# Kernel optimization log

Measured on AMD Instinct MI355X. Metric: run time of the kernel, lower is better.

Reference implementation:

```python
import jax, jax.numpy as jnp
import numpy as np

D_MODEL = 1024
NUM_HEADS = 16
HEAD_DIM = D_MODEL // NUM_HEADS  # 64


def setup_inputs() -> dict:
    key = jax.random.key(0)
    k1, k2, k3 = jax.random.split(key, 3)
    x = jax.random.normal(k1, (4, 2048, D_MODEL), dtype=jnp.float32)
    w_qkv = jax.random.normal(k2, (3 * D_MODEL, D_MODEL), dtype=jnp.float32) * 0.02
    b_qkv = jnp.zeros((3 * D_MODEL,), dtype=jnp.float32)
    w_out = jax.random.normal(k3, (D_MODEL, D_MODEL), dtype=jnp.float32) * 0.02
    b_out = jnp.zeros((D_MODEL,), dtype=jnp.float32)
    return {"x": x, "w_qkv": w_qkv, "b_qkv": b_qkv, "w_out": w_out, "b_out": b_out}


def reference(x, w_qkv, b_qkv, w_out, b_out):
    N, S, _ = x.shape
    # qkv projection: (N, S, 3*D) -> (3, N, heads, S, head_dim), matching torch permute(2,0,3,1,4)
    qkv = (jnp.einsum('nsd,ed->nse', x, w_qkv) + b_qkv)
    qkv = qkv.reshape(N, S, 3, NUM_HEADS, HEAD_DIM).transpose(2, 0, 3, 1, 4)
    queries, keys, values = qkv[0], qkv[1], qkv[2]  # each (N, heads, S, head_dim)
    # Faithful to source: einsum labels axis1 as 'q'/'k' and axis2 as 'h',
    # so energy has shape (N, S, heads, heads) -- attention over the heads axis.
    energy = jnp.einsum('nqhd,nkhd->nhqk', queries, keys)
    attention = jax.nn.softmax(energy / jnp.sqrt(jnp.float32(HEAD_DIM)), axis=3)
    out = jnp.einsum('nhql,nlhd->nqhd', attention, values).reshape(N, S, D_MODEL)
    return jnp.einsum('nsd,od->nso', out, w_out) + b_out
```

## Files before the change

### kernel.cpp

```cpp
#include <hip/hip_runtime.h>
#include <hip/hip_bf16.h>


typedef __hip_bfloat16 bf16;
using bf16x8 = __attribute__((ext_vector_type(8))) short;
using f32x4  = __attribute__((ext_vector_type(4))) float;

__device__ __forceinline__ float b2f(unsigned short u) {
    return __uint_as_float(((unsigned)u) << 16);
}
__device__ __forceinline__ unsigned short f2b(float f) {
    bf16 h = __float2bfloat16(f);
    return *reinterpret_cast<unsigned short*>(&h);
}
__device__ __forceinline__ void store1(float* p, float v) { *p = v; }
__device__ __forceinline__ void store1(bf16* p, float v) { *p = __float2bfloat16(v); }

__device__ __forceinline__ void gload_lds16(const bf16* g, bf16* l) {
    __builtin_amdgcn_global_load_lds(
        (const __attribute__((address_space(1))) void*)g,
        (__attribute__((address_space(3))) void*)l, 16, 0, 0);
}

#define BAR()   __builtin_amdgcn_s_barrier()
#define LGKM(N) asm volatile("s_waitcnt lgkmcnt(" #N ")" ::: "memory")
#define VMC(N)  asm volatile("s_waitcnt vmcnt(" #N ")" ::: "memory")

template <typename CT>
__global__ __launch_bounds__(512, 2)
void gemm3p(const bf16* __restrict__ A, const bf16* __restrict__ B,
            const float* __restrict__ bias, CT* __restrict__ C,
            int M, int N, int K, int gx) {
    __shared__ alignas(1024) bf16 smem[3][384 * 64];

    const int t    = threadIdx.x;
    const int lane = t & 63;
    const int wid  = t >> 6;
    const int wr   = wid >> 2;
    const int wc   = wid & 3;

    const int nwg = gridDim.x;
    const int bid = blockIdx.x;
    const int wg  = (bid & 7) * (nwg >> 3) + (bid >> 3);
    const int m0  = (wg / gx) * 128;
    const int n0  = (wg % gx) * 256;

    const int nt = K / 64;

    const int srow = lane >> 3;
    const int kel  = ((lane & 7) ^ (lane >> 3)) * 8;

    auto stageA = [&](int tt) {
        if (tt >= nt) return;
        bf16* lp = &smem[tt % 3][wid * 1024];
        const bf16* gp = A + (size_t)(m0 + wid * 16 + srow) * K + tt * 64 + kel;
        gload_lds16(gp, lp);
        gload_lds16(gp + (size_t)8 * K, lp + 512);
    };
    auto stageB = [&](int tt, int h) {
        if (tt >= nt) return;
        bf16* lp = &smem[tt % 3][8192 + h * 8192 + wid * 1024];
        const bf16* gp = B + (size_t)(n0 + h * 128 + wid * 16 + srow) * K + tt * 64 + kel;
        gload_lds16(gp, lp);
        gload_lds16(gp + (size_t)8 * K, lp + 512);
    };

    const int arow_base = wr * 64 + (lane & 15);
    const int brow_base = wc * 64 + (lane & 15);
    const int kqb       = (lane >> 4) * 16;
    auto LDA = [&](int buf, int kk, int m) -> bf16x8 {
        const int row = arow_base + m * 16;
        const int ab  = row * 128 + ((kk * 64 + kqb) ^ ((row & 7) << 4));
        return *(const bf16x8*)((const char*)&smem[buf][0] + ab);
    };
    auto LDB = [&](int buf, int kk, int n) -> bf16x8 {
        const int row = brow_base + n * 16;
        const int bb  = 16384 + row * 128 + ((kk * 64 + kqb) ^ ((row & 7) << 4));
        return *(const bf16x8*)((const char*)&smem[buf][0] + bb);
    };

    f32x4 acc[4][4] = {};
    bf16x8 afc[4], bfc[4];
    bf16x8 afa[4], bfa[4];

    stageA(0); stageB(0, 0); stageB(0, 1);
    stageA(1); stageB(1, 0); stageB(1, 1);
    VMC(6);
    BAR();
#pragma unroll
    for (int m = 0; m < 4; ++m) afc[m] = LDA(0, 0, m);
#pragma unroll
    for (int n = 0; n < 4; ++n) bfc[n] = LDB(0, 0, n);

    for (int tt = 0; tt < nt; ++tt) {
        const int buf = tt % 3;

#pragma unroll
        for (int m = 0; m < 4; ++m) afa[m] = LDA(buf, 1, m);
#pragma unroll
        for (int n = 0; n < 4; ++n) bfa[n] = LDB(buf, 1, n);
        stageA(tt + 2); stageB(tt + 2, 0); stageB(tt + 2, 1);
        LGKM(8);
        __builtin_amdgcn_s_setprio(1);
#pragma unroll
        for (int m = 0; m < 4; ++m)
#pragma unroll
            for (int n = 0; n < 4; ++n)
                acc[m][n] = __builtin_amdgcn_mfma_f32_16x16x32_bf16(
                    afc[m], bfc[n], acc[m][n], 0, 0, 0);
        __builtin_amdgcn_s_setprio(0);
        if (tt < nt - 2) { VMC(6); } else { VMC(0); }
        BAR();
        if (tt + 1 < nt) {
            const int nb = (tt + 1) % 3;
#pragma unroll
            for (int m = 0; m < 4; ++m) afc[m] = LDA(nb, 0, m);
#pragma unroll
            for (int n = 0; n < 4; ++n) bfc[n] = LDB(nb, 0, n);
            LGKM(8);
        } else {
            LGKM(0);
        }
        __builtin_amdgcn_s_setprio(1);
#pragma unroll
        for (int m = 0; m < 4; ++m)
#pragma unroll
            for (int n = 0; n < 4; ++n)
                acc[m][n] = __builtin_amdgcn_mfma_f32_16x16x32_bf16(
                    afa[m], bfa[n], acc[m][n], 0, 0, 0);
        __builtin_amdgcn_s_setprio(0);
        BAR();
    }

#pragma unroll
    for (int m = 0; m < 4; ++m) {
        const int row = m0 + wr * 64 + m * 16 + (lane >> 4) * 4;
#pragma unroll
        for (int n = 0; n < 4; ++n) {
            const int col = n0 + wc * 64 + n * 16 + (lane & 15);
            const float bval = bias[col];
#pragma unroll
            for (int r = 0; r < 4; ++r)
                store1(&C[(size_t)(row + r) * N + col], acc[m][n][r] + bval);
        }
    }
}

__global__ __launch_bounds__(256)
void cvt_f32_bf16(const float* __restrict__ in, bf16* __restrict__ out, int n4) {
    int i = blockIdx.x * 256 + threadIdx.x;
    if (i >= n4) return;
    float4 v = ((const float4*)in)[i];
    ushort4 o = {f2b(v.x), f2b(v.y), f2b(v.z), f2b(v.w)};
    ((ushort4*)out)[i] = o;
}

__global__ __launch_bounds__(256)
void attn_kernel(const bf16* __restrict__ qkv, bf16* __restrict__ T) {
    __shared__ float lds[4][48 * 68];

    const int wave = threadIdx.x >> 6;
    const int lane = threadIdx.x & 63;
    const int token = blockIdx.x * 4 + wave;
    const int n = token >> 11;
    const int s = token & 2047;

    float* L = lds[wave];
    const bf16* src = qkv + (size_t)token * 3072;

#pragma unroll
    for (int i = 0; i < 6; ++i) {
        int idx = i * 64 + lane;
        uint4 v = *reinterpret_cast<const uint4*>(src + (size_t)idx * 8);
        int e0 = idx * 8;
        float* dst = &L[(e0 >> 6) * 68 + (e0 & 63)];
        float4 a, b;
        a.x = b2f((unsigned short)(v.x & 0xffff));
        a.y = b2f((unsigned short)(v.x >> 16));
        a.z = b2f((unsigned short)(v.y & 0xffff));
        a.w = b2f((unsigned short)(v.y >> 16));
        b.x = b2f((unsigned short)(v.z & 0xffff));
        b.y = b2f((unsigned short)(v.z >> 16));
        b.z = b2f((unsigned short)(v.w & 0xffff));
        b.w = b2f((unsigned short)(v.w >> 16));
        *(float4*)dst = a;
        *(float4*)(dst + 4) = b;
    }
    __syncthreads();

    const int q0 = lane & 15;
    const int g  = lane >> 4;

    float e[4] = {0.f, 0.f, 0.f, 0.f};
    const float* Qr = &L[q0 * 68];
    const float* K0 = &L[(16 + g * 4) * 68];
#pragma unroll
    for (int d = 0; d < 64; d += 4) {
        float4 q4 = *(const float4*)(Qr + d);
#pragma unroll
        for (int j = 0; j < 4; ++j) {
            float4 k4 = *(const float4*)(K0 + j * 68 + d);
            e[j] += q4.x * k4.x + q4.y * k4.y + q4.z * k4.z + q4.w * k4.w;
        }
    }
#pragma unroll
    for (int j = 0; j < 4; ++j) e[j] *= 0.125f;

    float m = fmaxf(fmaxf(e[0], e[1]), fmaxf(e[2], e[3]));
    m = fmaxf(m, __shfl_xor(m, 16));
    m = fmaxf(m, __shfl_xor(m, 32));
    float p[4], sum = 0.f;
#pragma unroll
    for (int j = 0; j < 4; ++j) { p[j] = __expf(e[j] - m); sum += p[j]; }
    sum += __shfl_xor(sum, 16);
    sum += __shfl_xor(sum, 32);
    const float inv = 1.0f / sum;

    float prow[16];
#pragma unroll
    for (int j = 0; j < 4; ++j) {
        prow[g * 4 + j]         = p[j] * inv;
        prow[((g ^ 1) * 4) + j] = __shfl_xor(p[j], 16) * inv;
        prow[((g ^ 2) * 4) + j] = __shfl_xor(p[j], 32) * inv;
        prow[((g ^ 3) * 4) + j] = __shfl_xor(p[j], 48) * inv;
    }

    const int d0 = g * 16;
    float4 o4[4] = {};
#pragma unroll
    for (int k = 0; k < 16; ++k) {
        const float p1 = prow[k];
        const float* Vr = &L[(32 + k) * 68 + d0];
#pragma unroll
        for (int c = 0; c < 4; ++c) {
            float4 v = *(const float4*)(Vr + c * 4);
            o4[c].x += p1 * v.x; o4[c].y += p1 * v.y;
            o4[c].z += p1 * v.z; o4[c].w += p1 * v.w;
        }
    }
    unsigned short outv[16];
#pragma unroll
    for (int c = 0; c < 4; ++c) {
        outv[c * 4 + 0] = f2b(o4[c].x); outv[c * 4 + 1] = f2b(o4[c].y);
        outv[c * 4 + 2] = f2b(o4[c].z); outv[c * 4 + 3] = f2b(o4[c].w);
    }
    const int sp = q0 * 128 + (s >> 4);
    size_t off = ((size_t)n * 2048 + sp) * 1024 + (size_t)(s & 15) * 64 + d0;
    uint4* dst = reinterpret_cast<uint4*>(T + off);
    const uint4* sv = reinterpret_cast<const uint4*>(outv);
    dst[0] = sv[0];
    dst[1] = sv[1];
}

extern "C" void kernel_launch(void* const* d_in, const int* in_sizes, int n_in,
                              void* d_out, int out_size, void* d_ws, size_t ws_size,
                              hipStream_t stream) {
    const float* x     = (const float*)d_in[0];
    const float* w_qkv = (const float*)d_in[1];
    const float* b_qkv = (const float*)d_in[2];
    const float* w_out = (const float*)d_in[3];
    const float* b_out = (const float*)d_in[4];
    float* out = (float*)d_out;

    const int M = 8192, E = 3072, K = 1024, D = 1024;

    bf16* qkv = (bf16*)d_ws;
    bf16* T   = qkv + (size_t)M * E;
    bf16* W2b = qkv;
    bf16* W1b = (bf16*)d_out;
    bf16* X16 = W1b + (size_t)E * K;

    dim3 blk(256);

    cvt_f32_bf16<<<dim3(M * K / 4 / 256), blk, 0, stream>>>(x, X16, M * K / 4);
    cvt_f32_bf16<<<dim3(E * K / 4 / 256), blk, 0, stream>>>(w_qkv, W1b, E * K / 4);
    gemm3p<bf16><<<dim3((M / 128) * (E / 256)), dim3(512), 0, stream>>>(
        X16, W1b, b_qkv, qkv, M, E, K, E / 256);
    attn_kernel<<<dim3(M / 4), blk, 0, stream>>>(qkv, T);
    cvt_f32_bf16<<<dim3(D * K / 4 / 256), blk, 0, stream>>>(w_out, W2b, D * K / 4);
    gemm3p<float><<<dim3((M / 128) * (D / 256)), dim3(512), 0, stream>>>(
        T, W2b, b_out, out, M, D, K, D / 256);
}
```

Measured before the change: 127.9 us.

## Use one barrier per K-tile in GEMM and fuse the two input conversions

The GEMM main loop is restructured from two half-steps, each with its own barrier, to a single step per K tile. That step loads both k-halves of A and B fragments from LDS up front, then issues two MFMA batches with one barrier at the end. This removes a barrier and the cross-iteration fragment prefetch, trading load/compute overlap for less synchronization and more registers. Separately, the x and w_qkv fp32-to-bf16 conversions are merged into one launch to save a kernel launch.

```diff
diff --git a/kernel.cpp b/kernel.cpp
--- a/kernel.cpp
+++ b/kernel.cpp
@@ -28,7 +28,7 @@
 
 template <typename CT>
 __global__ __launch_bounds__(512, 2)
-void gemm3p(const bf16* __restrict__ A, const bf16* __restrict__ B,
+void gemm1b(const bf16* __restrict__ A, const bf16* __restrict__ B,
             const float* __restrict__ bias, CT* __restrict__ C,
             int M, int N, int K, int gx) {
     __shared__ alignas(1024) bf16 smem[3][384 * 64];
@@ -80,25 +80,24 @@
     };
 
     f32x4 acc[4][4] = {};
-    bf16x8 afc[4], bfc[4];
-    bf16x8 afa[4], bfa[4];
+    bf16x8 af0[4], bf0[4], af1[4], bf1[4];
 
     stageA(0); stageB(0, 0); stageB(0, 1);
     stageA(1); stageB(1, 0); stageB(1, 1);
     VMC(6);
     BAR();
-#pragma unroll
-    for (int m = 0; m < 4; ++m) afc[m] = LDA(0, 0, m);
-#pragma unroll
-    for (int n = 0; n < 4; ++n) bfc[n] = LDB(0, 0, n);
 
     for (int tt = 0; tt < nt; ++tt) {
         const int buf = tt % 3;
 
 #pragma unroll
-        for (int m = 0; m < 4; ++m) afa[m] = LDA(buf, 1, m);
-#pragma unroll
-        for (int n = 0; n < 4; ++n) bfa[n] = LDB(buf, 1, n);
+        for (int m = 0; m < 4; ++m) af0[m] = LDA(buf, 0, m);
+#pragma unroll
+        for (int n = 0; n < 4; ++n) bf0[n] = LDB(buf, 0, n);
+#pragma unroll
+        for (int m = 0; m < 4; ++m) af1[m] = LDA(buf, 1, m);
+#pragma unroll
+        for (int n = 0; n < 4; ++n) bf1[n] = LDB(buf, 1, n);
         stageA(tt + 2); stageB(tt + 2, 0); stageB(tt + 2, 1);
         LGKM(8);
         __builtin_amdgcn_s_setprio(1);
@@ -107,29 +106,19 @@
 #pragma unroll
             for (int n = 0; n < 4; ++n)
                 acc[m][n] = __builtin_amdgcn_mfma_f32_16x16x32_bf16(
-                    afc[m], bfc[n], acc[m][n], 0, 0, 0);
+                    af0[m], bf0[n], acc[m][n], 0, 0, 0);
+        __builtin_amdgcn_s_setprio(0);
+        LGKM(0);
+        __builtin_amdgcn_s_setprio(1);
+#pragma unroll
+        for (int m = 0; m < 4; ++m)
+#pragma unroll
+            for (int n = 0; n < 4; ++n)
+                acc[m][n] = __builtin_amdgcn_mfma_f32_16x16x32_bf16(
+                    af1[m], bf1[n], acc[m][n], 0, 0, 0);
         __builtin_amdgcn_s_setprio(0);
         if (tt < nt - 2) { VMC(6); } else { VMC(0); }
         BAR();
-        if (tt + 1 < nt) {
-            const int nb = (tt + 1) % 3;
-#pragma unroll
-            for (int m = 0; m < 4; ++m) afc[m] = LDA(nb, 0, m);
-#pragma unroll
-            for (int n = 0; n < 4; ++n) bfc[n] = LDB(nb, 0, n);
-            LGKM(8);
-        } else {
-            LGKM(0);
-        }
-        __builtin_amdgcn_s_setprio(1);
-#pragma unroll
-        for (int m = 0; m < 4; ++m)
-#pragma unroll
-            for (int n = 0; n < 4; ++n)
-                acc[m][n] = __builtin_amdgcn_mfma_f32_16x16x32_bf16(
-                    afa[m], bfa[n], acc[m][n], 0, 0, 0);
-        __builtin_amdgcn_s_setprio(0);
-        BAR();
     }
 
 #pragma unroll
@@ -144,6 +133,19 @@
                 store1(&C[(size_t)(row + r) * N + col], acc[m][n][r] + bval);
         }
     }
+}
+
+__global__ __launch_bounds__(256)
+void cvt2_f32_bf16(const float* __restrict__ in1, bf16* __restrict__ out1, int n1,
+                   const float* __restrict__ in2, bf16* __restrict__ out2, int n2) {
+    int i = blockIdx.x * 256 + threadIdx.x;
+    const float* in;
+    bf16* out;
+    if (i < n1) { in = in1; out = out1; }
+    else        { in = in2; out = out2; i -= n1; if (i >= n2) return; }
+    float4 v = ((const float4*)in)[i];
+    ushort4 o = {f2b(v.x), f2b(v.y), f2b(v.z), f2b(v.w)};
+    ((ushort4*)out)[i] = o;
 }
 
 __global__ __launch_bounds__(256)
@@ -271,13 +273,14 @@
     bf16* X16 = W1b + (size_t)E * K;
 
     dim3 blk(256);
-
-    cvt_f32_bf16<<<dim3(M * K / 4 / 256), blk, 0, stream>>>(x, X16, M * K / 4);
-    cvt_f32_bf16<<<dim3(E * K / 4 / 256), blk, 0, stream>>>(w_qkv, W1b, E * K / 4);
-    gemm3p<bf16><<<dim3((M / 128) * (E / 256)), dim3(512), 0, stream>>>(
+    const int n1 = M * K / 4, n2 = E * K / 4;
+
+    cvt2_f32_bf16<<<dim3((n1 + n2) / 256), blk, 0, stream>>>(
+        x, X16, n1, w_qkv, W1b, n2);
+    gemm1b<bf16><<<dim3((M / 128) * (E / 256)), dim3(512), 0, stream>>>(
         X16, W1b, b_qkv, qkv, M, E, K, E / 256);
     attn_kernel<<<dim3(M / 4), blk, 0, stream>>>(qkv, T);
     cvt_f32_bf16<<<dim3(D * K / 4 / 256), blk, 0, stream>>>(w_out, W2b, D * K / 4);
-    gemm3p<float><<<dim3((M / 128) * (D / 256)), dim3(512), 0, stream>>>(
+    gemm1b<float><<<dim3((M / 128) * (D / 256)), dim3(512), 0, stream>>>(
         T, W2b, b_out, out, M, D, K, D / 256);
 }
```

Result: faster. 124.1 us (-3.0%).

## Fuse fp32-to-bf16 conversion of x into QKV GEMM A-tile staging

Applied to the files above, without the earlier changes.

Drops the standalone conversion kernel for x. The QKV GEMM now loads fp32 A rows into registers, converts them to bf16 and writes them into swizzled LDS one stage ahead, while B still uses direct global-to-LDS loads. The main loop is also restructured so both k-halves are read from LDS at the start of each iteration, with one barrier per iteration instead of two. This removes a full write and re-read of the bf16 copy of x, at the cost of twice the global bytes for A, extra VALU conversion work and register pressure inside the GEMM.

```diff
diff --git a/kernel.cpp b/kernel.cpp
--- a/kernel.cpp
+++ b/kernel.cpp
@@ -26,11 +26,11 @@
 #define LGKM(N) asm volatile("s_waitcnt lgkmcnt(" #N ")" ::: "memory")
 #define VMC(N)  asm volatile("s_waitcnt vmcnt(" #N ")" ::: "memory")
 
-template <typename CT>
+template <bool AFP32, typename CT>
 __global__ __launch_bounds__(512, 2)
-void gemm3p(const bf16* __restrict__ A, const bf16* __restrict__ B,
-            const float* __restrict__ bias, CT* __restrict__ C,
-            int M, int N, int K, int gx) {
+void gemmf(const void* __restrict__ Av, const bf16* __restrict__ B,
+           const float* __restrict__ bias, CT* __restrict__ C,
+           int M, int N, int K, int gx) {
     __shared__ alignas(1024) bf16 smem[3][384 * 64];
 
     const int t    = threadIdx.x;
@@ -44,25 +44,53 @@
     const int wg  = (bid & 7) * (nwg >> 3) + (bid >> 3);
     const int m0  = (wg / gx) * 128;
     const int n0  = (wg % gx) * 256;
-
-    const int nt = K / 64;
+    const int nt  = K / 64;
 
     const int srow = lane >> 3;
     const int kel  = ((lane & 7) ^ (lane >> 3)) * 8;
 
-    auto stageA = [&](int tt) {
-        if (tt >= nt) return;
-        bf16* lp = &smem[tt % 3][wid * 1024];
-        const bf16* gp = A + (size_t)(m0 + wid * 16 + srow) * K + tt * 64 + kel;
-        gload_lds16(gp, lp);
-        gload_lds16(gp + (size_t)8 * K, lp + 512);
-    };
     auto stageB = [&](int tt, int h) {
         if (tt >= nt) return;
         bf16* lp = &smem[tt % 3][8192 + h * 8192 + wid * 1024];
         const bf16* gp = B + (size_t)(n0 + h * 128 + wid * 16 + srow) * K + tt * 64 + kel;
         gload_lds16(gp, lp);
         gload_lds16(gp + (size_t)8 * K, lp + 512);
+    };
+    auto stageA16 = [&](int tt) {
+        if (tt >= nt) return;
+        const bf16* A = (const bf16*)Av;
+        bf16* lp = &smem[tt % 3][wid * 1024];
+        const bf16* gp = A + (size_t)(m0 + wid * 16 + srow) * K + tt * 64 + kel;
+        gload_lds16(gp, lp);
+        gload_lds16(gp + (size_t)8 * K, lp + 512);
+    };
+
+    const int arow = t >> 2;
+    const int akb0 = (t & 3) * 32;
+    float4 ar0, ar1, ar2, ar3;
+    auto aregLoad = [&](int tt) {
+        if (tt >= nt) return;
+        const float* A = (const float*)Av;
+        const float* gp = A + (size_t)(m0 + arow) * K + tt * 64 + (akb0 >> 1);
+        ar0 = ((const float4*)gp)[0];
+        ar1 = ((const float4*)gp)[1];
+        ar2 = ((const float4*)gp)[2];
+        ar3 = ((const float4*)gp)[3];
+    };
+    auto aWriteF = [&](int tt, float4 f0, float4 f1, float4 f2, float4 f3) {
+        char* base = (char*)&smem[tt % 3][0];
+        const int swz = (arow & 7) << 4;
+        uint4 w0, w1;
+        w0.x = (unsigned)f2b(f0.x) | ((unsigned)f2b(f0.y) << 16);
+        w0.y = (unsigned)f2b(f0.z) | ((unsigned)f2b(f0.w) << 16);
+        w0.z = (unsigned)f2b(f1.x) | ((unsigned)f2b(f1.y) << 16);
+        w0.w = (unsigned)f2b(f1.z) | ((unsigned)f2b(f1.w) << 16);
+        w1.x = (unsigned)f2b(f2.x) | ((unsigned)f2b(f2.y) << 16);
+        w1.y = (unsigned)f2b(f2.z) | ((unsigned)f2b(f2.w) << 16);
+        w1.z = (unsigned)f2b(f3.x) | ((unsigned)f2b(f3.y) << 16);
+        w1.w = (unsigned)f2b(f3.z) | ((unsigned)f2b(f3.w) << 16);
+        *(uint4*)(base + arow * 128 + (akb0 ^ swz))        = w0;
+        *(uint4*)(base + arow * 128 + ((akb0 + 16) ^ swz)) = w1;
     };
 
     const int arow_base = wr * 64 + (lane & 15);
@@ -80,26 +108,54 @@
     };
 
     f32x4 acc[4][4] = {};
-    bf16x8 afc[4], bfc[4];
-    bf16x8 afa[4], bfa[4];
-
-    stageA(0); stageB(0, 0); stageB(0, 1);
-    stageA(1); stageB(1, 0); stageB(1, 1);
-    VMC(6);
-    BAR();
-#pragma unroll
-    for (int m = 0; m < 4; ++m) afc[m] = LDA(0, 0, m);
-#pragma unroll
-    for (int n = 0; n < 4; ++n) bfc[n] = LDB(0, 0, n);
+    bf16x8 af0[4], bv0[4], af1[4], bv1[4];
+
+    if constexpr (AFP32) {
+        stageB(0, 0); stageB(0, 1); stageB(1, 0); stageB(1, 1);
+        const float* A = (const float*)Av;
+        const float* g0 = A + (size_t)(m0 + arow) * K + (akb0 >> 1);
+        const float* g1 = g0 + 64;
+        float4 p0 = ((const float4*)g0)[0], p1 = ((const float4*)g0)[1],
+               p2 = ((const float4*)g0)[2], p3 = ((const float4*)g0)[3];
+        float4 q0 = ((const float4*)g1)[0], q1 = ((const float4*)g1)[1],
+               q2 = ((const float4*)g1)[2], q3 = ((const float4*)g1)[3];
+        VMC(0);
+        aWriteF(0, p0, p1, p2, p3);
+        aWriteF(1, q0, q1, q2, q3);
+        aregLoad(2);
+        LGKM(0);
+        BAR();
+    } else {
+        stageA16(0); stageB(0, 0); stageB(0, 1);
+        stageA16(1); stageB(1, 0); stageB(1, 1);
+        VMC(6);
+        BAR();
+    }
 
     for (int tt = 0; tt < nt; ++tt) {
         const int buf = tt % 3;
 
 #pragma unroll
-        for (int m = 0; m < 4; ++m) afa[m] = LDA(buf, 1, m);
-#pragma unroll
-        for (int n = 0; n < 4; ++n) bfa[n] = LDB(buf, 1, n);
-        stageA(tt + 2); stageB(tt + 2, 0); stageB(tt + 2, 1);
+        for (int m = 0; m < 4; ++m) af0[m] = LDA(buf, 0, m);
+#pragma unroll
+        for (int n = 0; n < 4; ++n) bv0[n] = LDB(buf, 0, n);
+#pragma unroll
+        for (int m = 0; m < 4; ++m) af1[m] = LDA(buf, 1, m);
+#pragma unroll
+        for (int n = 0; n < 4; ++n) bv1[n] = LDB(buf, 1, n);
+        stageB(tt + 2, 0); stageB(tt + 2, 1);
+        if constexpr (AFP32) {
+            if (tt + 2 < nt) {
+                VMC(4);
+                aWriteF(tt + 2, ar0, ar1, ar2, ar3);
+                aregLoad(tt + 3);
+            } else {
+                VMC(0);
+            }
+        } else {
+            stageA16(tt + 2);
+        }
+
         LGKM(8);
         __builtin_amdgcn_s_setprio(1);
 #pragma unroll
@@ -107,17 +163,10 @@
 #pragma unroll
             for (int n = 0; n < 4; ++n)
                 acc[m][n] = __builtin_amdgcn_mfma_f32_16x16x32_bf16(
-                    afc[m], bfc[n], acc[m][n], 0, 0, 0);
+                    af0[m], bv0[n], acc[m][n], 0, 0, 0);
         __builtin_amdgcn_s_setprio(0);
-        if (tt < nt - 2) { VMC(6); } else { VMC(0); }
-        BAR();
-        if (tt + 1 < nt) {
-            const int nb = (tt + 1) % 3;
-#pragma unroll
-            for (int m = 0; m < 4; ++m) afc[m] = LDA(nb, 0, m);
-#pragma unroll
-            for (int n = 0; n < 4; ++n) bfc[n] = LDB(nb, 0, n);
-            LGKM(8);
+        if constexpr (AFP32) {
+            if (tt + 2 < nt) { LGKM(2); } else { LGKM(0); }
         } else {
             LGKM(0);
         }
@@ -127,8 +176,14 @@
 #pragma unroll
             for (int n = 0; n < 4; ++n)
                 acc[m][n] = __builtin_amdgcn_mfma_f32_16x16x32_bf16(
-                    afa[m], bfa[n], acc[m][n], 0, 0, 0);
+                    af1[m], bv1[n], acc[m][n], 0, 0, 0);
         __builtin_amdgcn_s_setprio(0);
+
+        if constexpr (AFP32) {
+            LGKM(0);
+        } else {
+            if (tt < nt - 2) { VMC(6); } else { VMC(0); }
+        }
         BAR();
     }
 
@@ -268,16 +323,14 @@
     bf16* T   = qkv + (size_t)M * E;
     bf16* W2b = qkv;
     bf16* W1b = (bf16*)d_out;
-    bf16* X16 = W1b + (size_t)E * K;
 
     dim3 blk(256);
 
-    cvt_f32_bf16<<<dim3(M * K / 4 / 256), blk, 0, stream>>>(x, X16, M * K / 4);
     cvt_f32_bf16<<<dim3(E * K / 4 / 256), blk, 0, stream>>>(w_qkv, W1b, E * K / 4);
-    gemm3p<bf16><<<dim3((M / 128) * (E / 256)), dim3(512), 0, stream>>>(
-        X16, W1b, b_qkv, qkv, M, E, K, E / 256);
+    gemmf<true, bf16><<<dim3((M / 128) * (E / 256)), dim3(512), 0, stream>>>(
+        (const void*)x, W1b, b_qkv, qkv, M, E, K, E / 256);
     attn_kernel<<<dim3(M / 4), blk, 0, stream>>>(qkv, T);
     cvt_f32_bf16<<<dim3(D * K / 4 / 256), blk, 0, stream>>>(w_out, W2b, D * K / 4);
-    gemm3p<float><<<dim3((M / 128) * (D / 256)), dim3(512), 0, stream>>>(
-        T, W2b, b_out, out, M, D, K, D / 256);
-}
+    gemmf<false, float><<<dim3((M / 128) * (D / 256)), dim3(512), 0, stream>>>(
+        (const void*)T, W2b, b_out, out, M, D, K, D / 256);
+}
```

After: 148.1 us. 1.16x slower.
